# Kernel tuning notes

Measured on AMD Instinct MI355X. Metric: run time of the kernel, lower is better.

The kernel has to match this reference:

```python
import jax, jax.numpy as jnp
import numpy as np

N_NODES = 100000


def _graph_conv(x, src, dst, W, b):
    # DGL GraphConv, norm='both':
    # out = D_in^{-1/2} A D_out^{-1/2} x W + b, degrees clamped >= 1
    ones = jnp.ones(src.shape[0], dtype=x.dtype)
    deg_out = jax.ops.segment_sum(ones, src, num_segments=N_NODES)
    deg_in = jax.ops.segment_sum(ones, dst, num_segments=N_NODES)
    norm_src = jax.lax.rsqrt(jnp.maximum(deg_out, 1.0))  # [N]
    norm_dst = jax.lax.rsqrt(jnp.maximum(deg_in, 1.0))   # [N]
    h = x * norm_src[:, None]                    # [N, d_in]
    msg = h[src]                                 # [E, d_in] gather
    agg = jax.ops.segment_sum(msg, dst, num_segments=N_NODES)  # [N, d_in] scatter-add
    agg = agg * norm_dst[:, None]
    return agg @ W + b                           # [N, d_out]


def setup_inputs() -> dict:
    key = jax.random.key(0)
    k1, k2, k3, k4, k5 = jax.random.split(key, 5)
    n_edges = 1600000
    ndim, hdl, r = 32, 64, 32
    x = jax.random.normal(k1, (N_NODES, ndim), dtype=jnp.float32)
    src = jax.random.randint(k2, (n_edges,), 0, N_NODES, dtype=jnp.int32)
    dst = jax.random.randint(k3, (n_edges,), 0, N_NODES, dtype=jnp.int32)
    W1 = jax.random.normal(k4, (ndim, hdl), dtype=jnp.float32) / np.sqrt(ndim)
    b1 = jnp.zeros((hdl,), dtype=jnp.float32)
    W2 = jax.random.normal(k5, (hdl, r), dtype=jnp.float32) / np.sqrt(hdl)
    b2 = jnp.zeros((r,), dtype=jnp.float32)
    return {"x": x, "src": src, "dst": dst, "W1": W1, "b1": b1, "W2": W2, "b2": b2}


def reference(x, src, dst, W1, b1, W2, b2):
    z = _graph_conv(x, src, dst, W1, b1)
    z = _graph_conv(z, src, dst, W2, b2)
    return z
```

## Files before the change

### kernel.cpp

```cpp
#include <hip/hip_runtime.h>

#define N_NODES 100000
#define D_IN 32
#define D_HID 64
#define D_OUT 32
#define NBUCK 391
#define CHUNK 8192
#define CAP   8192

typedef unsigned short ushort8v __attribute__((ext_vector_type(8)));
typedef unsigned short ushort4v __attribute__((ext_vector_type(4)));

__device__ __forceinline__ float bf2f(unsigned short u) {
    return __uint_as_float((unsigned)u << 16);
}
__device__ __forceinline__ unsigned short f2bf(float f) {
    unsigned u = __float_as_uint(f);
    return (unsigned short)((u + 0x7FFF + ((u >> 16) & 1)) >> 16);
}

__global__ void zero_counts_kernel(int* __restrict__ p) {
    p[blockIdx.x * 256 + threadIdx.x] = 0;
}

__global__ __launch_bounds__(256) void bucket_hist_kernel(
    const int* __restrict__ src, const int* __restrict__ dst,
    int* __restrict__ sb_cnt, int* __restrict__ db_cnt, int E) {
    __shared__ int hs[NBUCK], hd[NBUCK];
    int tid = threadIdx.x;
    for (int i = tid; i < NBUCK; i += 256) { hs[i] = 0; hd[i] = 0; }
    __syncthreads();
    int stride = gridDim.x * 256;
    for (int e = blockIdx.x * 256 + tid; e < E; e += stride) {
        atomicAdd(&hs[src[e] >> 8], 1);
        atomicAdd(&hd[dst[e] >> 8], 1);
    }
    __syncthreads();
    for (int i = tid; i < NBUCK; i += 256) {
        if (hs[i]) atomicAdd(&sb_cnt[i], hs[i]);
        if (hd[i]) atomicAdd(&db_cnt[i], hd[i]);
    }
}

__global__ __launch_bounds__(512) void bucket_scan_kernel(
    const int* __restrict__ sb_cnt, const int* __restrict__ db_cnt,
    int* __restrict__ sb_base, int* __restrict__ db_base,
    int* __restrict__ sb_cur, int* __restrict__ db_cur, int E) {
    __shared__ int s[512];
    int tid = threadIdx.x;
    int v = (tid < NBUCK) ? sb_cnt[tid] : 0;
    s[tid] = v;
    __syncthreads();
    for (int off = 1; off < 512; off <<= 1) {
        int tv = (tid >= off) ? s[tid - off] : 0;
        __syncthreads(); s[tid] += tv; __syncthreads();
    }
    if (tid < NBUCK) { int e0 = s[tid] - v; sb_base[tid] = e0; sb_cur[tid] = e0; }
    if (tid == 0) sb_base[NBUCK] = E;
    __syncthreads();
    int v2 = (tid < NBUCK) ? db_cnt[tid] : 0;
    s[tid] = v2;
    __syncthreads();
    for (int off = 1; off < 512; off <<= 1) {
        int tv = (tid >= off) ? s[tid - off] : 0;
        __syncthreads(); s[tid] += tv; __syncthreads();
    }
    if (tid < NBUCK) { int e0 = s[tid] - v2; db_base[tid] = e0; db_cur[tid] = e0; }
    if (tid == 0) db_base[NBUCK] = E;
}

__global__ __launch_bounds__(512) void partition_both_kernel(
    const int* __restrict__ src, const int* __restrict__ dst,
    int* __restrict__ sb_cur, int* __restrict__ db_cur,
    int* __restrict__ ebuf, unsigned char* __restrict__ sbuf, int E) {
    __shared__ int dh[NBUCK], sh_[NBUCK];
    __shared__ int sarr[512];
    __shared__ int dloff[NBUCK], dgb[NBUCK], dcur[NBUCK];
    __shared__ int sloff[NBUCK], sgb[NBUCK], scur[NBUCK];
    __shared__ int dbuf[CHUNK];
    __shared__ unsigned char sbytes[CHUNK];
    int tid = threadIdx.x;
    int base = blockIdx.x * CHUNK;
    int lim = E - base; if (lim > CHUNK) lim = CHUNK;

    for (int i = tid; i < NBUCK; i += 512) { dh[i] = 0; sh_[i] = 0; }
    __syncthreads();
    for (int k = tid; k < lim; k += 512) {
        atomicAdd(&dh[dst[base + k] >> 8], 1);
        atomicAdd(&sh_[src[base + k] >> 8], 1);
    }
    __syncthreads();
    int v = (tid < NBUCK) ? dh[tid] : 0;
    sarr[tid] = v;
    __syncthreads();
    for (int off = 1; off < 512; off <<= 1) {
        int tv = (tid >= off) ? sarr[tid - off] : 0;
        __syncthreads(); sarr[tid] += tv; __syncthreads();
    }
    if (tid < NBUCK) {
        int excl = sarr[tid] - v;
        dloff[tid] = excl; dcur[tid] = excl;
        dgb[tid] = v ? atomicAdd(&db_cur[tid], v) : 0;
    }
    __syncthreads();
    int v2 = (tid < NBUCK) ? sh_[tid] : 0;
    sarr[tid] = v2;
    __syncthreads();
    for (int off = 1; off < 512; off <<= 1) {
        int tv = (tid >= off) ? sarr[tid - off] : 0;
        __syncthreads(); sarr[tid] += tv; __syncthreads();
    }
    if (tid < NBUCK) {
        int excl = sarr[tid] - v2;
        sloff[tid] = excl; scur[tid] = excl;
        sgb[tid] = v2 ? atomicAdd(&sb_cur[tid], v2) : 0;
    }
    __syncthreads();
    for (int k = tid; k < lim; k += 512) {
        int d = dst[base + k], s0 = src[base + k];
        int p = atomicAdd(&dcur[d >> 8], 1);
        dbuf[p] = (s0 << 8) | (d & 255);
        int p2 = atomicAdd(&scur[s0 >> 8], 1);
        sbytes[p2] = (unsigned char)(s0 & 255);
    }
    __syncthreads();
    int w = tid >> 6, lane = tid & 63;
    for (int b = w; b < NBUCK; b += 8) {
        int st = dloff[b], len = dh[b], gb = dgb[b];
        for (int i = lane; i < len; i += 64) ebuf[gb + i] = dbuf[st + i];
        int st2 = sloff[b], len2 = sh_[b], gb2 = sgb[b];
        for (int i = lane; i < len2; i += 64) sbuf[gb2 + i] = sbytes[st2 + i];
    }
}

__global__ __launch_bounds__(256) void bucket_finalize_kernel(
    const unsigned char* __restrict__ sbuf, const int* __restrict__ sb_base,
    const float4* __restrict__ x4, ushort4v* __restrict__ xs4b,
    float* __restrict__ norm_src,
    const int* __restrict__ ebuf, const int* __restrict__ db_base,
    int* __restrict__ rowptr, float* __restrict__ norm_dst,
    int* __restrict__ colidx, int n_nodes, int E) {
    __shared__ int limg[CAP];
    __shared__ int cnt[256];
    __shared__ int sc[256];
    __shared__ float nsl[256];
    int b = blockIdx.x, tid = threadIdx.x;
    int base_node = b << 8;
    int nn = n_nodes - base_node; if (nn > 256) nn = 256;

    int st = sb_base[b], en = sb_base[b + 1];
    cnt[tid] = 0;
    __syncthreads();
    for (int k = st + tid; k < en; k += 256) atomicAdd(&cnt[sbuf[k]], 1);
    __syncthreads();
    if (tid < nn) {
        int d = cnt[tid];
        float ns = rsqrtf((float)(d < 1 ? 1 : d));
        norm_src[base_node + tid] = ns;
        nsl[tid] = ns;
    }
    __syncthreads();
    for (int k = tid; k < nn * 8; k += 256) {
        float4 v = x4[((long)base_node << 3) + k];
        float s = nsl[k >> 3];
        ushort4v o;
        o[0] = f2bf(v.x * s); o[1] = f2bf(v.y * s);
        o[2] = f2bf(v.z * s); o[3] = f2bf(v.w * s);
        xs4b[((long)base_node << 3) + k] = o;
    }

    int cbase = db_base[b], cend = db_base[b + 1];
    int len = cend - cbase;
    __syncthreads();
    cnt[tid] = 0;
    __syncthreads();
    for (int k = tid; k < len; k += 256) atomicAdd(&cnt[ebuf[cbase + k] & 255], 1);
    __syncthreads();
    int v = cnt[tid];
    sc[tid] = v;
    __syncthreads();
    for (int off = 1; off < 256; off <<= 1) {
        int tv = (tid >= off) ? sc[tid - off] : 0;
        __syncthreads(); sc[tid] += tv; __syncthreads();
    }
    int excl = sc[tid] - v;
    if (tid < nn) {
        rowptr[base_node + tid] = cbase + excl;
        norm_dst[base_node + tid] = rsqrtf((float)(v < 1 ? 1 : v));
    }
    if (b == NBUCK - 1 && tid == 0) rowptr[n_nodes] = E;
    __syncthreads();
    cnt[tid] = excl;
    __syncthreads();
    if (len <= CAP) {
        for (int k = tid; k < len; k += 256) {
            int v2 = ebuf[cbase + k];
            int p = atomicAdd(&cnt[v2 & 255], 1);
            limg[p] = v2 >> 8;
        }
        __syncthreads();
        for (int k = tid; k < len; k += 256) colidx[cbase + k] = limg[k];
    } else {
        for (int k = tid; k < len; k += 256) {
            int v2 = ebuf[cbase + k];
            int p = atomicAdd(&cnt[v2 & 255], 1);
            colidx[cbase + p] = v2 >> 8;
        }
    }
}

__global__ __launch_bounds__(256) void gather1_kernel(
    const ushort8v* __restrict__ xs8, const int* __restrict__ colidx,
    const int* __restrict__ rowptr, float* __restrict__ agg, int n_nodes) {
    int t = threadIdx.x;
    int w = t >> 6, lane = t & 63;
    int quarter = lane >> 4, ql = lane & 15;
    int eh = ql >> 2, q = ql & 3;
    int qb = quarter << 4;
    int nquads = (n_nodes + 3) >> 2;

    for (int p = blockIdx.x * 4 + w; p < nquads; p += gridDim.x * 4) {
        int base_node = p << 2;
        int idx = base_node + lane;
        if (idx > n_nodes) idx = n_nodes;
        int rr = (lane < 5) ? rowptr[idx] : 0;
        int myS = __shfl(rr, quarter);
        int myE = __shfl(rr, quarter + 1);
        int myD = myE - myS;
        int dm = myD;
        dm = max(dm, __shfl_xor(dm, 16));
        dm = max(dm, __shfl_xor(dm, 32));
        float a[8];
#pragma unroll
        for (int r = 0; r < 8; ++r) a[r] = 0.f;
        for (int base = 0; base < dm; base += 16) {
            int mylim = myD - base; mylim = mylim < 0 ? 0 : (mylim > 16 ? 16 : mylim);
            int c_reg = (ql < mylim) ? colidx[myS + base + ql] : 0;
            int c0 = __shfl(c_reg, qb | eh);
            int c1 = __shfl(c_reg, qb | (eh + 4));
            int c2 = __shfl(c_reg, qb | (eh + 8));
            int c3 = __shfl(c_reg, qb | (eh + 12));
            ushort8v v0 = xs8[(long)c0 * 4 + q];
            ushort8v v1 = xs8[(long)c1 * 4 + q];
            ushort8v v2 = xs8[(long)c2 * 4 + q];
            ushort8v v3 = xs8[(long)c3 * 4 + q];
            float m0 = (eh      < mylim) ? 1.f : 0.f;
            float m1 = (eh +  4 < mylim) ? 1.f : 0.f;
            float m2 = (eh +  8 < mylim) ? 1.f : 0.f;
            float m3 = (eh + 12 < mylim) ? 1.f : 0.f;
#pragma unroll
            for (int r = 0; r < 8; ++r) {
                a[r] = fmaf(bf2f(v0[r]), m0, a[r]);
                a[r] = fmaf(bf2f(v1[r]), m1, a[r]);
                a[r] = fmaf(bf2f(v2[r]), m2, a[r]);
                a[r] = fmaf(bf2f(v3[r]), m3, a[r]);
            }
        }
#pragma unroll
        for (int r = 0; r < 8; ++r) { a[r] += __shfl_xor(a[r], 4); a[r] += __shfl_xor(a[r], 8); }
        if (ql < 4) {
            int n_ = base_node + quarter;
            if (n_ < n_nodes) {
                float* orow = agg + (long)n_ * 32 + ql * 8;
                float4 o1, o2;
                o1.x = a[0]; o1.y = a[1]; o1.z = a[2]; o1.w = a[3];
                o2.x = a[4]; o2.y = a[5]; o2.z = a[6]; o2.w = a[7];
                ((float4*)orow)[0] = o1;
                ((float4*)orow)[1] = o2;
            }
        }
    }
}

__global__ __launch_bounds__(256) void gemm_fused_kernel(
    const float* __restrict__ agg, const float* __restrict__ norm_src,
    const float* __restrict__ norm_dst,
    const float* __restrict__ W1, const float* __restrict__ b1,
    const float* __restrict__ W2, unsigned short* __restrict__ ybf, int n_nodes) {
    __shared__ float W1s[D_IN * D_HID];
    __shared__ float W2s[D_HID * D_OUT];
    __shared__ float b1s[D_HID];
    __shared__ float accs[4][2][D_IN];
    __shared__ float z1s[4][2][D_HID];
    int t = threadIdx.x;
    for (int i = t; i < 2048; i += 256) { W1s[i] = W1[i]; W2s[i] = W2[i]; }
    if (t < D_HID) b1s[t] = b1[t];
    __syncthreads();
    int w = t >> 6, lane = t & 63;
    int half = lane >> 5, hl = lane & 31;
    int npairs = (n_nodes + 1) >> 1;
    for (int p = blockIdx.x * 4 + w; p < npairs; p += gridDim.x * 4) {
        int nA = 2 * p, nB = nA + 1;
        bool hasB = nB < n_nodes;
        int nh = half ? (hasB ? nB : nA) : nA;
        accs[w][half][hl] = agg[(long)nh * 32 + hl];
        float ndA = norm_dst[nA], ndB = hasB ? norm_dst[nB] : 0.f;
        float s1A = 0.f, s1B = 0.f;
#pragma unroll
        for (int k = 0; k < D_IN; ++k) {
            float wv = W1s[k * D_HID + lane];
            s1A = fmaf(accs[w][0][k], wv, s1A);
            s1B = fmaf(accs[w][1][k], wv, s1B);
        }
        z1s[w][0][lane] = ndA * s1A + b1s[lane];
        z1s[w][1][lane] = ndB * s1B + b1s[lane];
        float s2 = 0.f;
#pragma unroll
        for (int k = 0; k < D_HID; ++k) s2 = fmaf(z1s[w][half][k], W2s[k * D_OUT + hl], s2);
        int n_ = half ? nB : nA;
        if (!half || hasB) ybf[(long)n_ * 32 + hl] = f2bf(norm_src[n_] * s2);
    }
}

__global__ __launch_bounds__(256) void gather2_kernel(
    const ushort8v* __restrict__ y8, const int* __restrict__ colidx,
    const int* __restrict__ rowptr, const float* __restrict__ norm_dst,
    const float* __restrict__ b2, float* __restrict__ out, int n_nodes) {
    int t = threadIdx.x;
    int w = t >> 6, lane = t & 63;
    int quarter = lane >> 4, ql = lane & 15;
    int eh = ql >> 2, q = ql & 3;
    int qb = quarter << 4;
    int nquads = (n_nodes + 3) >> 2;

    for (int p = blockIdx.x * 4 + w; p < nquads; p += gridDim.x * 4) {
        int base_node = p << 2;
        int idx = base_node + lane;
        if (idx > n_nodes) idx = n_nodes;
        int rr = (lane < 5) ? rowptr[idx] : 0;
        int myS = __shfl(rr, quarter);
        int myE = __shfl(rr, quarter + 1);
        int myD = myE - myS;
        int dm = myD;
        dm = max(dm, __shfl_xor(dm, 16));
        dm = max(dm, __shfl_xor(dm, 32));
        float a[8];
#pragma unroll
        for (int r = 0; r < 8; ++r) a[r] = 0.f;
        for (int base = 0; base < dm; base += 16) {
            int mylim = myD - base; mylim = mylim < 0 ? 0 : (mylim > 16 ? 16 : mylim);
            int c_reg = (ql < mylim) ? colidx[myS + base + ql] : 0;
            int c0 = __shfl(c_reg, qb | eh);
            int c1 = __shfl(c_reg, qb | (eh + 4));
            int c2 = __shfl(c_reg, qb | (eh + 8));
            int c3 = __shfl(c_reg, qb | (eh + 12));
            ushort8v v0 = y8[(long)c0 * 4 + q];
            ushort8v v1 = y8[(long)c1 * 4 + q];
            ushort8v v2 = y8[(long)c2 * 4 + q];
            ushort8v v3 = y8[(long)c3 * 4 + q];
            float m0 = (eh      < mylim) ? 1.f : 0.f;
            float m1 = (eh +  4 < mylim) ? 1.f : 0.f;
            float m2 = (eh +  8 < mylim) ? 1.f : 0.f;
            float m3 = (eh + 12 < mylim) ? 1.f : 0.f;
#pragma unroll
            for (int r = 0; r < 8; ++r) {
                a[r] = fmaf(bf2f(v0[r]), m0, a[r]);
                a[r] = fmaf(bf2f(v1[r]), m1, a[r]);
                a[r] = fmaf(bf2f(v2[r]), m2, a[r]);
                a[r] = fmaf(bf2f(v3[r]), m3, a[r]);
            }
        }
#pragma unroll
        for (int r = 0; r < 8; ++r) { a[r] += __shfl_xor(a[r], 4); a[r] += __shfl_xor(a[r], 8); }
        if (ql < 4) {
            int n_ = base_node + quarter;
            if (n_ < n_nodes) {
                float nd = norm_dst[n_];
                const float4 bL = ((const float4*)b2)[ql * 2];
                const float4 bH = ((const float4*)b2)[ql * 2 + 1];
                float4 o1, o2;
                o1.x = fmaf(a[0], nd, bL.x); o1.y = fmaf(a[1], nd, bL.y);
                o1.z = fmaf(a[2], nd, bL.z); o1.w = fmaf(a[3], nd, bL.w);
                o2.x = fmaf(a[4], nd, bH.x); o2.y = fmaf(a[5], nd, bH.y);
                o2.z = fmaf(a[6], nd, bH.z); o2.w = fmaf(a[7], nd, bH.w);
                float* orow = out + (long)n_ * 32 + ql * 8;
                ((float4*)orow)[0] = o1;
                ((float4*)orow)[1] = o2;
            }
        }
    }
}

extern "C" void kernel_launch(void* const* d_in, const int* in_sizes, int n_in,
                              void* d_out, int out_size, void* d_ws, size_t ws_size,
                              hipStream_t stream) {
    const float* x   = (const float*)d_in[0];
    const int*   src = (const int*)d_in[1];
    const int*   dst = (const int*)d_in[2];
    const float* W1  = (const float*)d_in[3];
    const float* b1  = (const float*)d_in[4];
    const float* W2  = (const float*)d_in[5];
    const float* b2  = (const float*)d_in[6];

    const int N = N_NODES;
    const int E = in_sizes[1];

    int* ws_i    = (int*)d_ws;
    int* sb_cnt  = ws_i;
    int* db_cnt  = ws_i + 512;
    int* sb_base = ws_i + 1024;
    int* db_base = ws_i + 1536;
    int* sb_cur  = ws_i + 2048;
    int* db_cur  = ws_i + 2560;
    int* rowptr  = ws_i + 3072;
    int* colidx  = ws_i + 103104;
    float* norms = (float*)(ws_i + 1703104);
    int* ebuf    = ws_i + 1903104;
    unsigned char* sbuf = (unsigned char*)(ws_i + 3503104);
    unsigned short* xsb = (unsigned short*)(ws_i + 3903104);
    float* agg   = (float*)(ws_i + 5503104);
    unsigned short* ybf = (unsigned short*)ebuf;

    zero_counts_kernel<<<4, 256, 0, stream>>>(ws_i);

    bucket_hist_kernel<<<256, 256, 0, stream>>>(src, dst, sb_cnt, db_cnt, E);
    bucket_scan_kernel<<<1, 512, 0, stream>>>(sb_cnt, db_cnt, sb_base, db_base,
                                              sb_cur, db_cur, E);

    int pb = (E + CHUNK - 1) / CHUNK;
    partition_both_kernel<<<pb, 512, 0, stream>>>(src, dst, sb_cur, db_cur,
                                                  ebuf, sbuf, E);
    bucket_finalize_kernel<<<NBUCK, 256, 0, stream>>>(sbuf, sb_base,
                                                      (const float4*)x, (ushort4v*)xsb,
                                                      norms, ebuf, db_base, rowptr,
                                                      norms + N, colidx, N, E);

    gather1_kernel<<<2048, 256, 0, stream>>>((const ushort8v*)xsb, colidx, rowptr,
                                             agg, N);
    gemm_fused_kernel<<<2048, 256, 0, stream>>>(agg, norms, norms + N,
                                                W1, b1, W2, ybf, N);
    gather2_kernel<<<2048, 256, 0, stream>>>((const ushort8v*)ybf, colidx, rowptr,
                                             norms + N, b2, (float*)d_out, N);
}
```

Baseline: 163.2 us.

## Sort nodes by in-degree so gather wavefronts process similar-degree rows

Builds a degree histogram during finalize, scans it, and computes a permutation of nodes grouped by in-degree (capped at 255). Both gather kernels then process nodes in permuted order, so each wavefront's four nodes have similar degree, which cuts the masked idle lanes caused by taking the max degree across the quad. It adds two small kernels and an extra indirection through perm, and output writes become scattered rather than contiguous. It also reuses sb_cnt as the degree-bin buffer after the scan zeroes it.

```diff
diff --git a/kernel.cpp b/kernel.cpp
--- a/kernel.cpp
+++ b/kernel.cpp
@@ -43,7 +43,7 @@
 }
 
 __global__ __launch_bounds__(512) void bucket_scan_kernel(
-    const int* __restrict__ sb_cnt, const int* __restrict__ db_cnt,
+    int* __restrict__ sb_cnt, const int* __restrict__ db_cnt,
     int* __restrict__ sb_base, int* __restrict__ db_base,
     int* __restrict__ sb_cur, int* __restrict__ db_cur, int E) {
     __shared__ int s[512];
@@ -67,6 +67,8 @@
     }
     if (tid < NBUCK) { int e0 = s[tid] - v2; db_base[tid] = e0; db_cur[tid] = e0; }
     if (tid == 0) db_base[NBUCK] = E;
+    __syncthreads();
+    sb_cnt[tid] = 0;
 }
 
 __global__ __launch_bounds__(512) void partition_both_kernel(
@@ -139,17 +141,19 @@
     float* __restrict__ norm_src,
     const int* __restrict__ ebuf, const int* __restrict__ db_base,
     int* __restrict__ rowptr, float* __restrict__ norm_dst,
-    int* __restrict__ colidx, int n_nodes, int E) {
+    int* __restrict__ colidx, int* __restrict__ dbins, int n_nodes, int E) {
     __shared__ int limg[CAP];
     __shared__ int cnt[256];
     __shared__ int sc[256];
     __shared__ float nsl[256];
+    __shared__ int dbh[256];
     int b = blockIdx.x, tid = threadIdx.x;
     int base_node = b << 8;
     int nn = n_nodes - base_node; if (nn > 256) nn = 256;
 
     int st = sb_base[b], en = sb_base[b + 1];
     cnt[tid] = 0;
+    dbh[tid] = 0;
     __syncthreads();
     for (int k = st + tid; k < en; k += 256) atomicAdd(&cnt[sbuf[k]], 1);
     __syncthreads();
@@ -187,9 +191,11 @@
     if (tid < nn) {
         rowptr[base_node + tid] = cbase + excl;
         norm_dst[base_node + tid] = rsqrtf((float)(v < 1 ? 1 : v));
+        atomicAdd(&dbh[v < 255 ? v : 255], 1);
     }
     if (b == NBUCK - 1 && tid == 0) rowptr[n_nodes] = E;
     __syncthreads();
+    if (dbh[tid]) atomicAdd(&dbins[tid], dbh[tid]);
     cnt[tid] = excl;
     __syncthreads();
     if (len <= CAP) {
@@ -209,9 +215,35 @@
     }
 }
 
+__global__ __launch_bounds__(256) void deg_scan_kernel(int* __restrict__ bins) {
+    __shared__ int s[256];
+    int tid = threadIdx.x;
+    int v = bins[tid];
+    s[tid] = v;
+    __syncthreads();
+    for (int off = 1; off < 256; off <<= 1) {
+        int tv = (tid >= off) ? s[tid - off] : 0;
+        __syncthreads(); s[tid] += tv; __syncthreads();
+    }
+    bins[tid] = s[tid] - v;
+}
+
+__global__ __launch_bounds__(256) void place_perm_kernel(
+    const int* __restrict__ rowptr, int* __restrict__ cursor,
+    int* __restrict__ perm, int n_nodes) {
+    int n = blockIdx.x * 256 + threadIdx.x;
+    if (n < n_nodes) {
+        int d = rowptr[n + 1] - rowptr[n];
+        int b = d < 255 ? d : 255;
+        int p = atomicAdd(&cursor[b], 1);
+        perm[p] = n;
+    }
+}
+
 __global__ __launch_bounds__(256) void gather1_kernel(
     const ushort8v* __restrict__ xs8, const int* __restrict__ colidx,
-    const int* __restrict__ rowptr, float* __restrict__ agg, int n_nodes) {
+    const int* __restrict__ rowptr, const int* __restrict__ perm,
+    float* __restrict__ agg, int n_nodes) {
     int t = threadIdx.x;
     int w = t >> 6, lane = t & 63;
     int quarter = lane >> 4, ql = lane & 15;
@@ -220,13 +252,11 @@
     int nquads = (n_nodes + 3) >> 2;
 
     for (int p = blockIdx.x * 4 + w; p < nquads; p += gridDim.x * 4) {
-        int base_node = p << 2;
-        int idx = base_node + lane;
-        if (idx > n_nodes) idx = n_nodes;
-        int rr = (lane < 5) ? rowptr[idx] : 0;
-        int myS = __shfl(rr, quarter);
-        int myE = __shfl(rr, quarter + 1);
-        int myD = myE - myS;
+        int nidx = (p << 2) + quarter;
+        bool valid = nidx < n_nodes;
+        int node = valid ? perm[nidx] : 0;
+        int myS = rowptr[node];
+        int myD = valid ? rowptr[node + 1] - myS : 0;
         int dm = myD;
         dm = max(dm, __shfl_xor(dm, 16));
         dm = max(dm, __shfl_xor(dm, 32));
@@ -258,16 +288,13 @@
         }
 #pragma unroll
         for (int r = 0; r < 8; ++r) { a[r] += __shfl_xor(a[r], 4); a[r] += __shfl_xor(a[r], 8); }
-        if (ql < 4) {
-            int n_ = base_node + quarter;
-            if (n_ < n_nodes) {
-                float* orow = agg + (long)n_ * 32 + ql * 8;
-                float4 o1, o2;
-                o1.x = a[0]; o1.y = a[1]; o1.z = a[2]; o1.w = a[3];
-                o2.x = a[4]; o2.y = a[5]; o2.z = a[6]; o2.w = a[7];
-                ((float4*)orow)[0] = o1;
-                ((float4*)orow)[1] = o2;
-            }
+        if (ql < 4 && valid) {
+            float* orow = agg + (long)node * 32 + ql * 8;
+            float4 o1, o2;
+            o1.x = a[0]; o1.y = a[1]; o1.z = a[2]; o1.w = a[3];
+            o2.x = a[4]; o2.y = a[5]; o2.z = a[6]; o2.w = a[7];
+            ((float4*)orow)[0] = o1;
+            ((float4*)orow)[1] = o2;
         }
     }
 }
@@ -314,7 +341,8 @@
 
 __global__ __launch_bounds__(256) void gather2_kernel(
     const ushort8v* __restrict__ y8, const int* __restrict__ colidx,
-    const int* __restrict__ rowptr, const float* __restrict__ norm_dst,
+    const int* __restrict__ rowptr, const int* __restrict__ perm,
+    const float* __restrict__ norm_dst,
     const float* __restrict__ b2, float* __restrict__ out, int n_nodes) {
     int t = threadIdx.x;
     int w = t >> 6, lane = t & 63;
@@ -324,13 +352,11 @@
     int nquads = (n_nodes + 3) >> 2;
 
     for (int p = blockIdx.x * 4 + w; p < nquads; p += gridDim.x * 4) {
-        int base_node = p << 2;
-        int idx = base_node + lane;
-        if (idx > n_nodes) idx = n_nodes;
-        int rr = (lane < 5) ? rowptr[idx] : 0;
-        int myS = __shfl(rr, quarter);
-        int myE = __shfl(rr, quarter + 1);
-        int myD = myE - myS;
+        int nidx = (p << 2) + quarter;
+        bool valid = nidx < n_nodes;
+        int node = valid ? perm[nidx] : 0;
+        int myS = rowptr[node];
+        int myD = valid ? rowptr[node + 1] - myS : 0;
         int dm = myD;
         dm = max(dm, __shfl_xor(dm, 16));
         dm = max(dm, __shfl_xor(dm, 32));
@@ -362,21 +388,18 @@
         }
 #pragma unroll
         for (int r = 0; r < 8; ++r) { a[r] += __shfl_xor(a[r], 4); a[r] += __shfl_xor(a[r], 8); }
-        if (ql < 4) {
-            int n_ = base_node + quarter;
-            if (n_ < n_nodes) {
-                float nd = norm_dst[n_];
-                const float4 bL = ((const float4*)b2)[ql * 2];
-                const float4 bH = ((const float4*)b2)[ql * 2 + 1];
-                float4 o1, o2;
-                o1.x = fmaf(a[0], nd, bL.x); o1.y = fmaf(a[1], nd, bL.y);
-                o1.z = fmaf(a[2], nd, bL.z); o1.w = fmaf(a[3], nd, bL.w);
-                o2.x = fmaf(a[4], nd, bH.x); o2.y = fmaf(a[5], nd, bH.y);
-                o2.z = fmaf(a[6], nd, bH.z); o2.w = fmaf(a[7], nd, bH.w);
-                float* orow = out + (long)n_ * 32 + ql * 8;
-                ((float4*)orow)[0] = o1;
-                ((float4*)orow)[1] = o2;
-            }
+        if (ql < 4 && valid) {
+            float nd = norm_dst[node];
+            const float4 bL = ((const float4*)b2)[ql * 2];
+            const float4 bH = ((const float4*)b2)[ql * 2 + 1];
+            float4 o1, o2;
+            o1.x = fmaf(a[0], nd, bL.x); o1.y = fmaf(a[1], nd, bL.y);
+            o1.z = fmaf(a[2], nd, bL.z); o1.w = fmaf(a[3], nd, bL.w);
+            o2.x = fmaf(a[4], nd, bH.x); o2.y = fmaf(a[5], nd, bH.y);
+            o2.z = fmaf(a[6], nd, bH.z); o2.w = fmaf(a[7], nd, bH.w);
+            float* orow = out + (long)node * 32 + ql * 8;
+            ((float4*)orow)[0] = o1;
+            ((float4*)orow)[1] = o2;
         }
     }
 }
@@ -409,6 +432,7 @@
     unsigned char* sbuf = (unsigned char*)(ws_i + 3503104);
     unsigned short* xsb = (unsigned short*)(ws_i + 3903104);
     float* agg   = (float*)(ws_i + 5503104);
+    int* perm    = ws_i + 8703104;
     unsigned short* ybf = (unsigned short*)ebuf;
 
     zero_counts_kernel<<<4, 256, 0, stream>>>(ws_i);
@@ -423,12 +447,15 @@
     bucket_finalize_kernel<<<NBUCK, 256, 0, stream>>>(sbuf, sb_base,
                                                       (const float4*)x, (ushort4v*)xsb,
                                                       norms, ebuf, db_base, rowptr,
-                                                      norms + N, colidx, N, E);
+                                                      norms + N, colidx, sb_cnt, N, E);
+
+    deg_scan_kernel<<<1, 256, 0, stream>>>(sb_cnt);
+    place_perm_kernel<<<NBUCK, 256, 0, stream>>>(rowptr, sb_cnt, perm, N);
 
     gather1_kernel<<<2048, 256, 0, stream>>>((const ushort8v*)xsb, colidx, rowptr,
-                                             agg, N);
+                                             perm, agg, N);
     gemm_fused_kernel<<<2048, 256, 0, stream>>>(agg, norms, norms + N,
                                                 W1, b1, W2, ybf, N);
     gather2_kernel<<<2048, 256, 0, stream>>>((const ushort8v*)ybf, colidx, rowptr,
-                                             norms + N, b2, (float*)d_out, N);
-}
+                                             perm, norms + N, b2, (float*)d_out, N);
+}
```

After: 433.7 us. 2.66x slower.
